# Optimization experiments

Measured on AMD Instinct MI355X. Metric: run time of the kernel, lower is better.

The kernel has to match this reference:

```python
import jax, jax.numpy as jnp
import numpy as np

EPS_KERAS = 1e-7  # keras backend epsilon used by SparseCategoricalCrossentropy clipping


def _box_terms(p_boxes, g_boxes):
    # boxes are cxcywh; module uses pixel-style '+1' widths. Returns (iou, bg_ratio).
    p_ul = p_boxes[..., :2] - 0.5 * p_boxes[..., 2:]
    p_dr = p_boxes[..., :2] + 0.5 * p_boxes[..., 2:]
    g_ul = g_boxes[..., :2] - 0.5 * g_boxes[..., 2:]
    g_dr = g_boxes[..., :2] + 0.5 * g_boxes[..., 2:]
    inter_wh = jnp.maximum(jnp.minimum(p_dr, g_dr) - jnp.maximum(p_ul, g_ul) + 1.0, 0.0)
    inter = inter_wh[..., 0] * inter_wh[..., 1]
    p_wh = jnp.maximum(p_dr - p_ul + 1.0, 0.0)
    g_wh = jnp.maximum(g_dr - g_ul + 1.0, 0.0)
    p_area = p_wh[..., 0] * p_wh[..., 1]
    g_area = g_wh[..., 0] * g_wh[..., 1]
    union = p_area + g_area - inter
    iou = inter / jnp.maximum(union, 1e-9)
    bound_wh = jnp.maximum(jnp.maximum(p_dr, g_dr) - jnp.minimum(p_ul, g_ul) + 1.0, 0.0)
    bound = bound_wh[..., 0] * bound_wh[..., 1]
    bg_ratio = (bound - union) / jnp.maximum(bound, 1e-9)
    return iou, bg_ratio


def _cost_matrix(bbox_pred, labels_pred, bbox_gt, labels_gt):
    # Vectorized over batch: [B,Q,G] pairwise L1 + (-GIoU) + (-prob of gt class)
    bp = bbox_pred[:, :, None, :]   # [B,Q,1,4]
    bg = bbox_gt[:, None, :, :]     # [B,1,G,4]
    l1 = jnp.sum(jnp.abs(bp - bg), axis=-1)
    iou, bg_ratio = _box_terms(bp, bg)
    B, Q, _ = labels_pred.shape
    G = labels_gt.shape[1]
    idx = jnp.broadcast_to(labels_gt[:, None, :].astype(jnp.int32), (B, Q, G))
    probs = jnp.take_along_axis(labels_pred, idx, axis=2)
    return l1 - (iou - bg_ratio) - probs


def _hungarian(cost):
    # Exact min-cost assignment for a square matrix (Jonker-Volgenant style,
    # e-maxx Hungarian). Host-side, mirrors scipy.optimize.linear_sum_assignment.
    cost = np.asarray(cost, dtype=np.float64)
    n = cost.shape[0]
    u = np.zeros(n + 1)
    v = np.zeros(n + 1)
    p = np.zeros(n + 1, dtype=np.int64)    # p[j]: row matched to column j (1-based)
    way = np.zeros(n + 1, dtype=np.int64)
    for i in range(1, n + 1):
        p[0] = i
        j0 = 0
        minv = np.full(n + 1, np.inf)
        used = np.zeros(n + 1, dtype=bool)
        while True:
            used[j0] = True
            i0 = p[j0]
            cur = cost[i0 - 1] - u[i0] - v[1:]
            free = ~used[1:]
            better = free & (cur < minv[1:])
            minv[1:][better] = cur[better]
            way[1:][better] = j0
            masked = np.where(free, minv[1:], np.inf)
            j1 = int(np.argmin(masked)) + 1
            delta = masked[j1 - 1]
            uidx = np.nonzero(used)[0]
            u[p[uidx]] += delta
            v[uidx] -= delta
            minv[~used] -= delta
            j0 = j1
            if p[j0] == 0:
                break
        while j0 != 0:
            j1 = way[j0]
            p[j0] = p[j1]
            j0 = j1
    ans = np.zeros(n, dtype=np.int64)
    ans[p[1:] - 1] = np.arange(n)   # ans[row] = matched col
    return ans


def _losses(bbox_pred, labels_pred, bbox_gt, labels_gt, col):
    # col: [B,Q] matched gt column per query (row_ind is arange for square cost).
    # Label loss: scatter of matched gt labels onto queries == gather by col,
    # then keras SparseCategoricalCrossentropy(from_logits=False):
    # clip probs to [eps,1-eps], log, softmax-CE (== -log p for normalized probs).
    query_labels = jnp.take_along_axis(labels_gt.astype(jnp.int32), col, axis=1)  # [B,Q]
    logits = jnp.log(jnp.clip(labels_pred, EPS_KERAS, 1.0 - EPS_KERAS))
    logp = jax.nn.log_softmax(logits, axis=-1)
    nll = -jnp.take_along_axis(logp, query_labels[..., None], axis=-1)[..., 0]    # [B,Q]
    label_loss = jnp.mean(nll, axis=1)
    # Bbox L1: pred rows gathered by arange (identity), gt gathered by col.
    target = jnp.take_along_axis(bbox_gt, col[..., None], axis=1)                 # [B,Q,4]
    reg_loss = jnp.mean(jnp.abs(bbox_pred - target), axis=(1, 2))
    # GIoU term: original code uses UN-permuted gt here (faithful to source),
    # and adds +mean(iou - bg_ratio) (sign as in source).
    iou, bg_ratio = _box_terms(bbox_pred, bbox_gt)
    giou = jnp.mean(iou - bg_ratio, axis=1)
    per_sample = 1.0 * label_loss + 5.0 * reg_loss + 2.0 * giou
    return jnp.sum(per_sample)


def reference(bbox_pred, labels_pred, bbox_gt, labels_gt):
    cost = np.asarray(_cost_matrix(bbox_pred, labels_pred, bbox_gt, labels_gt))
    col = jnp.asarray(np.stack([_hungarian(c) for c in cost]))  # [B,Q]
    return _losses(bbox_pred, labels_pred, bbox_gt, labels_gt, col)


def setup_inputs() -> dict:
    key = jax.random.key(0)
    k1, k2, k3, k4 = jax.random.split(key, 4)
    B, Q, G, C = 16, 100, 100, 100
    bbox_pred = jax.random.uniform(k1, (B, Q, 4), dtype=jnp.float32)
    labels_pred = jax.nn.softmax(jax.random.normal(k2, (B, Q, C), dtype=jnp.float32), axis=-1)
    bbox_gt = jax.random.uniform(k3, (B, G, 4), dtype=jnp.float32)
    labels_gt = jax.random.randint(k4, (B, G), 0, C, dtype=jnp.int32)
    return {"bbox_pred": bbox_pred, "labels_pred": labels_pred, "bbox_gt": bbox_gt, "labels_gt": labels_gt}
```

## Files before the change

### kernel.cpp

```cpp
#include <hip/hip_runtime.h>
#include <math.h>

#define NB 100

__device__ __forceinline__ void box_terms(const float bp[4], const float bg[4],
                                          float &iou, float &bgr) {
    float p_ul0 = bp[0] - 0.5f * bp[2], p_ul1 = bp[1] - 0.5f * bp[3];
    float p_dr0 = bp[0] + 0.5f * bp[2], p_dr1 = bp[1] + 0.5f * bp[3];
    float g_ul0 = bg[0] - 0.5f * bg[2], g_ul1 = bg[1] - 0.5f * bg[3];
    float g_dr0 = bg[0] + 0.5f * bg[2], g_dr1 = bg[1] + 0.5f * bg[3];
    float iw0 = fmaxf(fminf(p_dr0, g_dr0) - fmaxf(p_ul0, g_ul0) + 1.0f, 0.0f);
    float iw1 = fmaxf(fminf(p_dr1, g_dr1) - fmaxf(p_ul1, g_ul1) + 1.0f, 0.0f);
    float inter = iw0 * iw1;
    float pw0 = fmaxf(p_dr0 - p_ul0 + 1.0f, 0.0f);
    float pw1 = fmaxf(p_dr1 - p_ul1 + 1.0f, 0.0f);
    float gw0 = fmaxf(g_dr0 - g_ul0 + 1.0f, 0.0f);
    float gw1 = fmaxf(g_dr1 - g_ul1 + 1.0f, 0.0f);
    float pa = pw0 * pw1, ga = gw0 * gw1;
    float uni = pa + ga - inter;
    iou = inter / fmaxf(uni, 1e-9f);
    float bw0 = fmaxf(fmaxf(p_dr0, g_dr0) - fminf(p_ul0, g_ul0) + 1.0f, 0.0f);
    float bw1 = fmaxf(fmaxf(p_dr1, g_dr1) - fminf(p_ul1, g_ul1) + 1.0f, 0.0f);
    float bound = bw0 * bw1;
    bgr = (bound - uni) / fmaxf(bound, 1e-9f);
}

template<int CTRL>
__device__ __forceinline__ double dpp_f64(double x) {
    int lo = __builtin_amdgcn_update_dpp(0, __double2loint(x), CTRL, 0xF, 0xF, true);
    int hi = __builtin_amdgcn_update_dpp(0, __double2hiint(x), CTRL, 0xF, 0xF, true);
    return __hiloint2double(hi, lo);
}

template<int CTRL>
__device__ __forceinline__ double dpp_f64_keep(double x) {
    int lo = __builtin_amdgcn_update_dpp(__double2loint(x), __double2loint(x),
                                         CTRL, 0xF, 0xF, false);
    int hi = __builtin_amdgcn_update_dpp(__double2hiint(x), __double2hiint(x),
                                         CTRL, 0xF, 0xF, false);
    return __hiloint2double(hi, lo);
}

__device__ __forceinline__ double readlane_f64(double x, int l) {
    int lo = __builtin_amdgcn_readlane(__double2loint(x), l);
    int hi = __builtin_amdgcn_readlane(__double2hiint(x), l);
    return __hiloint2double(hi, lo);
}

__device__ __forceinline__ double wave_min_f64(double x) {
    double q1 = dpp_f64<0xB1>(x);
    double q2 = dpp_f64<0x4E>(x);
    double q3 = dpp_f64<0x1B>(x);
    x = fmin(fmin(x, q1), fmin(q2, q3));
    double h1 = dpp_f64<0x141>(x);
    double h2 = dpp_f64<0x140>(x);
    double h3 = dpp_f64_keep<0x118>(x);
    x = fmin(fmin(x, h1), fmin(h2, h3));
    x = fmin(x, dpp_f64<0x142>(x));
    x = fmin(x, dpp_f64<0x143>(x));
    return readlane_f64(x, 63);
}

__device__ __forceinline__ double wave_min_packed(double x, int &lo_out) {
    double q1 = dpp_f64<0xB1>(x);
    double q2 = dpp_f64<0x4E>(x);
    double q3 = dpp_f64<0x1B>(x);
    x = fmin(fmin(x, q1), fmin(q2, q3));
    double h1 = dpp_f64<0x141>(x);
    double h2 = dpp_f64<0x140>(x);
    double h3 = dpp_f64_keep<0x118>(x);
    x = fmin(fmin(x, h1), fmin(h2, h3));
    x = fmin(x, dpp_f64<0x142>(x));
    x = fmin(x, dpp_f64<0x143>(x));
    int lo = __builtin_amdgcn_readlane(__double2loint(x), 63);
    int hi = __builtin_amdgcn_readlane(__double2hiint(x), 63);
    lo_out = lo;
    return __hiloint2double(hi, lo);
}

__device__ __forceinline__ double pack_tag(double g, int tag) {
    unsigned long long bi = (unsigned long long)__double_as_longlong(g);
    bi = (bi & ~0x3FFFULL) | (unsigned long long)(unsigned)tag;
    return __longlong_as_double((long long)bi);
}

__global__ __launch_bounds__(256) void fused_match_loss(
    const float* __restrict__ bbox_pred,
    const float* __restrict__ labels_pred,
    const float* __restrict__ bbox_gt,
    const int*   __restrict__ labels_gt,
    float* __restrict__ out)
{
    __shared__ float  cost_sh[NB * NB + 64];
    __shared__ double u_sh[NB];
    __shared__ double v_sh[NB];
    __shared__ int    rowclaim_sh[NB];
    __shared__ int    col_sh[NB];
    __shared__ float  bp_sh[NB * 4];
    __shared__ float  bg_sh[NB * 4];
    __shared__ int    lg_sh[NB];
    __shared__ float  lse_sh[NB];
    __shared__ float  gio_sh[NB];
    __shared__ float  red_sh[3 * 128];

    const int b = blockIdx.x;
    const int t = threadIdx.x;
    const int lane = t & 63;
    const bool hasB = (lane + 64 < NB);
    const double QNAN = __longlong_as_double(0x7FF8000000000000LL);
    const float* lp = labels_pred + (size_t)b * NB * NB;

    double vA = 0.0, vB = 0.0;
    double uA = 0.0, uB = 0.0;
    int pA = -1, pB = -1;
    unsigned long long remLo = 0, remHi = 0;

    for (int i = t; i < NB * 4; i += 256) {
        bp_sh[i] = bbox_pred[(size_t)b * NB * 4 + i];
        bg_sh[i] = bbox_gt[(size_t)b * NB * 4 + i];
    }
    for (int i = t; i < NB; i += 256) {
        lg_sh[i] = labels_gt[b * NB + i];
        rowclaim_sh[i] = 0x7FFFFFFF;
    }
    __syncthreads();

    for (int idx = t; idx < NB * NB; idx += 256) {
        int q = idx / NB, g = idx - q * NB;
        float bp[4] = {bp_sh[q*4+0], bp_sh[q*4+1], bp_sh[q*4+2], bp_sh[q*4+3]};
        float bg[4] = {bg_sh[g*4+0], bg_sh[g*4+1], bg_sh[g*4+2], bg_sh[g*4+3]};
        float l1 = fabsf(bp[0]-bg[0]) + fabsf(bp[1]-bg[1])
                 + fabsf(bp[2]-bg[2]) + fabsf(bp[3]-bg[3]);
        float iou, bgr;
        box_terms(bp, bg, iou, bgr);
        float prob = lp[q * NB + lg_sh[g]];
        cost_sh[idx] = l1 - (iou - bgr) - prob;
    }
    __syncthreads();

    if (t < 64) {
        float bestA = INFINITY, bestB = INFINITY;
        int iminA = 0, iminB = 0;
        for (int i = 0; i < NB; ++i) {
            float cA = cost_sh[i * NB + lane];
            float cB = cost_sh[i * NB + lane + 64];
            if (cA < bestA) { bestA = cA; iminA = i; }
            if (hasB && cB < bestB) { bestB = cB; iminB = i; }
        }
        atomicMin(&rowclaim_sh[iminA], lane);
        if (hasB) atomicMin(&rowclaim_sh[iminB], lane + 64);

        vA = (double)bestA;
        vB = hasB ? (double)bestB : 0.0;
        v_sh[lane] = vA;
        if (hasB) v_sh[lane + 64] = vB;
        pA = (rowclaim_sh[iminA] == lane) ? iminA : -1;
        pB = (hasB && rowclaim_sh[iminB] == lane + 64) ? iminB : -1;
        remLo = __ballot(rowclaim_sh[lane] == 0x7FFFFFFF);
        remHi = __ballot(hasB && rowclaim_sh[lane + 64] == 0x7FFFFFFF);
    }
    __syncthreads();

    {
        const int w = t >> 6;
        for (int i = w; i < NB; i += 4) {
            double r = (double)cost_sh[i * NB + lane] - v_sh[lane];
            if (hasB)
                r = fmin(r, (double)cost_sh[i * NB + lane + 64] - v_sh[lane + 64]);
            r = wave_min_f64(r);
            if (lane == 0)
                u_sh[i] = (rowclaim_sh[i] != 0x7FFFFFFF) ? 0.0 : r;
        }
    }
    __syncthreads();

    if (t < 64) {
        {
            unsigned long long gLo = remLo, gHi = remHi;
            while (gLo | gHi) {
                int i;
                if (gLo) { i = __ffsll((long long)gLo) - 1; gLo &= gLo - 1; }
                else { i = 64 + __ffsll((long long)gHi) - 1; gHi &= gHi - 1; }
                double u_i = u_sh[i];
                const float* crow = &cost_sh[i * NB];
                double rdA = (double)crow[lane] - u_i - vA;
                double rdB = (double)crow[lane + 64] - u_i - vB;
                unsigned long long ba = __ballot(pA < 0 && rdA == 0.0);
                unsigned long long bb = __ballot(hasB && pB < 0 && rdB == 0.0);
                if (ba) {
                    int wl = __ffsll((long long)ba) - 1;
                    if (lane == wl) { pA = i; uA = u_i; }
                } else if (bb) {
                    int wl = __ffsll((long long)bb) - 1;
                    if (lane == wl) { pB = i; uB = u_i; }
                } else continue;
                if (i < 64) remLo &= ~(1ull << i); else remHi &= ~(1ull << (i - 64));
            }
        }

        auto phase = [&](int irow) {
            double GAq = QNAN, GBq = QNAN;
            int wayA = -1, wayB = -1;
            bool usedA = false, usedB = !hasB;
            double DusedA = 0.0, DusedB = 0.0;
            double D = 0.0;
            int jprevmark = -1;
            double u0 = u_sh[irow];
            double Df; int jfin;

            const int tagA = ((pA + 1) << 7) | lane;
            const int tagB = ((pB + 1) << 7) | (lane + 64);

            float cA = cost_sh[irow * NB + lane];
            float cB = cost_sh[irow * NB + lane + 64];

            for (;;) {
                double du = D - u0;
                double candAq = pack_tag(((double)cA - vA) + du, tagA);
                if (!usedA && !(candAq >= GAq)) { GAq = candAq; wayA = jprevmark; }
                double candBq = pack_tag(((double)cB - vB) + du, tagB);
                if (!usedB && !(candBq >= GBq)) { GBq = candBq; wayB = jprevmark; }
                int wlo;
                const double m = wave_min_packed(fmin(GAq, GBq), wlo);
                const int j1 = wlo & 0x7F;
                const int prow = ((wlo >> 7) & 0x7F) - 1;
                const bool isA = (j1 < 64);
                const int winLane = j1 & 63;
                if (prow < 0) { Df = m; jfin = j1; break; }
                cA = cost_sh[prow * NB + lane];
                cB = cost_sh[prow * NB + lane + 64];
                double unext = readlane_f64(isA ? uA : uB, winLane);
                if (lane == winLane) {
                    if (isA) { usedA = true; DusedA = m; GAq = QNAN; }
                    else     { usedB = true; DusedB = m; GBq = QNAN; }
                }
                u0 = unext; jprevmark = j1; D = m;
            }

            if (usedA) { uA += Df - DusedA; vA -= Df - DusedA; }
            if (hasB && usedB) { uB += Df - DusedB; vB -= Df - DusedB; }

            int jcur = jfin;
            while (jcur != -1) {
                int wl = jcur & 63;
                int jprev = (jcur < 64) ? __builtin_amdgcn_readlane(wayA, wl)
                                        : __builtin_amdgcn_readlane(wayB, wl);
                int row; double unew;
                if (jprev < 0) { row = irow; unew = u_sh[irow] + Df; }
                else {
                    int pl = jprev & 63;
                    int rA = __builtin_amdgcn_readlane(pA, pl);
                    int rB = __builtin_amdgcn_readlane(pB, pl);
                    double xA = readlane_f64(uA, pl);
                    double xB = readlane_f64(uB, pl);
                    row  = (jprev < 64) ? rA : rB;
                    unew = (jprev < 64) ? xA : xB;
                }
                if (jcur < 64) { if (lane == jcur)      { pA = row; uA = unew; } }
                else           { if (lane == jcur - 64) { pB = row; uB = unew; } }
                jcur = jprev;
            }
        };

        while (remLo) { int i = __ffsll((long long)remLo) - 1; remLo &= remLo - 1; phase(i); }
        while (remHi) { int i = 64 + __ffsll((long long)remHi) - 1; remHi &= remHi - 1; phase(i); }

        if (pA >= 0) col_sh[pA] = lane;
        if (hasB && pB >= 0) col_sh[pB] = lane + 64;
    } else {
        const int q = t - 64;
        if (q < NB) {
            const float* row = lp + q * NB;
            const float hi = 1.0f - 1e-7f;
            float mx = -INFINITY;
            for (int k = 0; k < NB; ++k) {
                float lg = logf(fminf(fmaxf(row[k], 1e-7f), hi));
                mx = fmaxf(mx, lg);
            }
            float se = 0.0f;
            for (int k = 0; k < NB; ++k) {
                float lg = logf(fminf(fmaxf(row[k], 1e-7f), hi));
                se += expf(lg - mx);
            }
            lse_sh[q] = mx + logf(se);

            float bp[4] = {bp_sh[q*4+0], bp_sh[q*4+1], bp_sh[q*4+2], bp_sh[q*4+3]};
            float bq[4] = {bg_sh[q*4+0], bg_sh[q*4+1], bg_sh[q*4+2], bg_sh[q*4+3]};
            float iou, bgr;
            box_terms(bp, bq, iou, bgr);
            gio_sh[q] = iou - bgr;
        }
    }
    __syncthreads();

    float nll = 0.0f, regsum = 0.0f, giou = 0.0f;
    if (t < NB) {
        const int q = t;
        const int cg = col_sh[q];
        const int cidx = lg_sh[cg];
        const float hi = 1.0f - 1e-7f;
        float logit_c = logf(fminf(fmaxf(lp[q * NB + cidx], 1e-7f), hi));
        nll = lse_sh[q] - logit_c;

        for (int k = 0; k < 4; ++k)
            regsum += fabsf(bp_sh[q*4+k] - bg_sh[cg*4+k]);

        giou = gio_sh[q];
    }
    if (t < 128) {
        red_sh[t]       = nll;
        red_sh[128 + t] = regsum;
        red_sh[256 + t] = giou;
    }
    __syncthreads();
    if (t < 64) {
        float a = red_sh[t]       + red_sh[t + 64];
        float r = red_sh[128 + t] + red_sh[128 + t + 64];
        float g = red_sh[256 + t] + red_sh[256 + t + 64];
        #pragma unroll
        for (int off = 32; off > 0; off >>= 1) {
            a += __shfl_xor(a, off, 64);
            r += __shfl_xor(r, off, 64);
            g += __shfl_xor(g, off, 64);
        }
        if (t == 0) {
            float ps = a * (1.0f / NB) + 5.0f * (r * (1.0f / (NB * 4)))
                     + 2.0f * (g * (1.0f / NB));
            atomicAdd(out, ps);
        }
    }
}

extern "C" void kernel_launch(void* const* d_in, const int* in_sizes, int n_in,
                              void* d_out, int out_size, void* d_ws, size_t ws_size,
                              hipStream_t stream) {
    const float* bbox_pred   = (const float*)d_in[0];
    const float* labels_pred = (const float*)d_in[1];
    const float* bbox_gt     = (const float*)d_in[2];
    const int*   labels_gt   = (const int*)d_in[3];
    float* out = (float*)d_out;

    const int B = in_sizes[0] / (NB * 4);

    fused_match_loss<<<B, 256, 0, stream>>>(bbox_pred, labels_pred, bbox_gt,
                                            labels_gt, out);
}
```

Measured before the change: 359.1 us.

## Store cost matrix as double in LDS and track row potentials in shared memory

Widens the shared cost matrix from float to double so the Hungarian inner loop can skip float-to-double conversions. Row potentials are now read from a shared u array indexed by row, replacing a cross-lane readlane of the column's potential. Per-column used-distances go to a shared array instead of per-lane registers. The used-column marking sets only the high word to NaN. This doubles LDS footprint to about 80KB, which may reduce occupancy or exceed limits, and adds extra shared stores inside the serial augmenting loop.

```diff
diff --git a/kernel.cpp b/kernel.cpp
--- a/kernel.cpp
+++ b/kernel.cpp
@@ -91,9 +91,10 @@
     const int*   __restrict__ labels_gt,
     float* __restrict__ out)
 {
-    __shared__ float  cost_sh[NB * NB + 64];
+    __shared__ double cost_sh[NB * NB + 64];
     __shared__ double u_sh[NB];
     __shared__ double v_sh[NB];
+    __shared__ double dused_sh[NB];
     __shared__ int    rowclaim_sh[NB];
     __shared__ int    col_sh[NB];
     __shared__ float  bp_sh[NB * 4];
@@ -134,24 +135,24 @@
         float iou, bgr;
         box_terms(bp, bg, iou, bgr);
         float prob = lp[q * NB + lg_sh[g]];
-        cost_sh[idx] = l1 - (iou - bgr) - prob;
+        cost_sh[idx] = (double)(l1 - (iou - bgr) - prob);
     }
     __syncthreads();
 
     if (t < 64) {
-        float bestA = INFINITY, bestB = INFINITY;
+        double bestA = (double)INFINITY, bestB = (double)INFINITY;
         int iminA = 0, iminB = 0;
         for (int i = 0; i < NB; ++i) {
-            float cA = cost_sh[i * NB + lane];
-            float cB = cost_sh[i * NB + lane + 64];
+            double cA = cost_sh[i * NB + lane];
+            double cB = cost_sh[i * NB + lane + 64];
             if (cA < bestA) { bestA = cA; iminA = i; }
             if (hasB && cB < bestB) { bestB = cB; iminB = i; }
         }
         atomicMin(&rowclaim_sh[iminA], lane);
         if (hasB) atomicMin(&rowclaim_sh[iminB], lane + 64);
 
-        vA = (double)bestA;
-        vB = hasB ? (double)bestB : 0.0;
+        vA = bestA;
+        vB = hasB ? bestB : 0.0;
         v_sh[lane] = vA;
         if (hasB) v_sh[lane + 64] = vB;
         pA = (rowclaim_sh[iminA] == lane) ? iminA : -1;
@@ -164,9 +165,9 @@
     {
         const int w = t >> 6;
         for (int i = w; i < NB; i += 4) {
-            double r = (double)cost_sh[i * NB + lane] - v_sh[lane];
+            double r = cost_sh[i * NB + lane] - v_sh[lane];
             if (hasB)
-                r = fmin(r, (double)cost_sh[i * NB + lane + 64] - v_sh[lane + 64]);
+                r = fmin(r, cost_sh[i * NB + lane + 64] - v_sh[lane + 64]);
             r = wave_min_f64(r);
             if (lane == 0)
                 u_sh[i] = (rowclaim_sh[i] != 0x7FFFFFFF) ? 0.0 : r;
@@ -182,9 +183,9 @@
                 if (gLo) { i = __ffsll((long long)gLo) - 1; gLo &= gLo - 1; }
                 else { i = 64 + __ffsll((long long)gHi) - 1; gHi &= gHi - 1; }
                 double u_i = u_sh[i];
-                const float* crow = &cost_sh[i * NB];
-                double rdA = (double)crow[lane] - u_i - vA;
-                double rdB = (double)crow[lane + 64] - u_i - vB;
+                const double* crow = &cost_sh[i * NB];
+                double rdA = crow[lane] - u_i - vA;
+                double rdB = crow[lane + 64] - u_i - vB;
                 unsigned long long ba = __ballot(pA < 0 && rdA == 0.0);
                 unsigned long long bb = __ballot(hasB && pB < 0 && rdB == 0.0);
                 if (ba) {
@@ -202,7 +203,6 @@
             double GAq = QNAN, GBq = QNAN;
             int wayA = -1, wayB = -1;
             bool usedA = false, usedB = !hasB;
-            double DusedA = 0.0, DusedB = 0.0;
             double D = 0.0;
             int jprevmark = -1;
             double u0 = u_sh[irow];
@@ -211,14 +211,14 @@
             const int tagA = ((pA + 1) << 7) | lane;
             const int tagB = ((pB + 1) << 7) | (lane + 64);
 
-            float cA = cost_sh[irow * NB + lane];
-            float cB = cost_sh[irow * NB + lane + 64];
+            double cA = cost_sh[irow * NB + lane];
+            double cB = cost_sh[irow * NB + lane + 64];
 
             for (;;) {
                 double du = D - u0;
-                double candAq = pack_tag(((double)cA - vA) + du, tagA);
+                double candAq = pack_tag((cA - vA) + du, tagA);
                 if (!usedA && !(candAq >= GAq)) { GAq = candAq; wayA = jprevmark; }
-                double candBq = pack_tag(((double)cB - vB) + du, tagB);
+                double candBq = pack_tag((cB - vB) + du, tagB);
                 if (!usedB && !(candBq >= GBq)) { GBq = candBq; wayB = jprevmark; }
                 int wlo;
                 const double m = wave_min_packed(fmin(GAq, GBq), wlo);
@@ -229,16 +229,30 @@
                 if (prow < 0) { Df = m; jfin = j1; break; }
                 cA = cost_sh[prow * NB + lane];
                 cB = cost_sh[prow * NB + lane + 64];
-                double unext = readlane_f64(isA ? uA : uB, winLane);
+                double unext = u_sh[prow];
                 if (lane == winLane) {
-                    if (isA) { usedA = true; DusedA = m; GAq = QNAN; }
-                    else     { usedB = true; DusedB = m; GBq = QNAN; }
+                    dused_sh[j1] = m;
+                    if (isA) {
+                        usedA = true;
+                        GAq = __hiloint2double(0x7FF80000, __double2loint(GAq));
+                    } else {
+                        usedB = true;
+                        GBq = __hiloint2double(0x7FF80000, __double2loint(GBq));
+                    }
                 }
                 u0 = unext; jprevmark = j1; D = m;
             }
 
-            if (usedA) { uA += Df - DusedA; vA -= Df - DusedA; }
-            if (hasB && usedB) { uB += Df - DusedB; vB -= Df - DusedB; }
+            if (usedA) {
+                double DusedA = dused_sh[lane];
+                uA += Df - DusedA; vA -= Df - DusedA;
+            }
+            if (hasB && usedB) {
+                double DusedB = dused_sh[lane + 64];
+                uB += Df - DusedB; vB -= Df - DusedB;
+            }
+            if (usedA) u_sh[pA] = uA;
+            if (hasB && usedB) u_sh[pB] = uB;
 
             int jcur = jfin;
             while (jcur != -1) {
@@ -246,8 +260,10 @@
                 int jprev = (jcur < 64) ? __builtin_amdgcn_readlane(wayA, wl)
                                         : __builtin_amdgcn_readlane(wayB, wl);
                 int row; double unew;
-                if (jprev < 0) { row = irow; unew = u_sh[irow] + Df; }
-                else {
+                if (jprev < 0) {
+                    row = irow; unew = u_sh[irow] + Df;
+                    if (lane == 0) u_sh[irow] = unew;
+                } else {
                     int pl = jprev & 63;
                     int rA = __builtin_amdgcn_readlane(pA, pl);
                     int rB = __builtin_amdgcn_readlane(pB, pl);
```

Result: slower. 376.9 us (+5.0%).
